# Kernel tuning notes

Measured on AMD Instinct MI355X. Metric: run time of the kernel, lower is better.

Reference implementation:

```python
import jax, jax.numpy as jnp
import numpy as np

B, N, D, J, L = 8, 2046, 128, 128, 2  # batch, ops, feature len, jobs, blocks
C = N + 2  # ops + appended begin/end rows


def setup_inputs() -> dict:
    key = jax.random.key(0)
    ks = jax.random.split(key, 40)

    def w(k, shape, fan_in):
        return jax.random.normal(k, shape, jnp.float32) / np.float32(np.sqrt(fan_in))

    inp = {}
    inp["operation_features"] = jax.random.normal(ks[0], (B, N, D), jnp.float32)
    inp["same_type_mask"] = (jax.random.uniform(ks[1], (B, N, N)) > 0.5).astype(jnp.float32)
    inp["relations"] = jax.random.randint(ks[2], (B, N, 2), 0, N, jnp.int32)
    inp["begins_idx"] = jax.random.randint(ks[3], (B, J), 0, N, jnp.int32)
    inp["ends_idx"] = jax.random.randint(ks[4], (B, J), 0, N, jnp.int32)
    # begin_end_init params
    inp["init_bp_w"] = w(ks[5], (D, D), D); inp["init_bp_b"] = jnp.zeros((D,), jnp.float32)
    inp["init_ep_w"] = w(ks[6], (D, D), D); inp["init_ep_b"] = jnp.zeros((D,), jnp.float32)
    # per-block params, stacked on leading L axis
    inp["be_bp_w"] = w(ks[7], (L, D, D), D); inp["be_bp_b"] = jnp.zeros((L, D), jnp.float32)
    inp["be_ep_w"] = w(ks[8], (L, D, D), D); inp["be_ep_b"] = jnp.zeros((L, D), jnp.float32)
    inp["seq_mix_w"] = w(ks[9], (L, 3 * D, D), 3 * D); inp["seq_mix_b"] = jnp.zeros((L, D), jnp.float32)
    inp["attn_w_w"] = w(ks[10], (L, D, 3 * D), D); inp["attn_w_b"] = jnp.zeros((L, 3 * D), jnp.float32)
    inp["score_w"] = w(ks[11], (L, 2 * D), 2 * D); inp["score_b"] = jnp.zeros((L,), jnp.float32)
    inp["attn_out_w"] = w(ks[12], (L, D, D), D); inp["attn_out_b"] = jnp.zeros((L, D), jnp.float32)
    inp["mix_w"] = w(ks[13], (L, 2 * D, D), 2 * D); inp["mix_b"] = jnp.zeros((L, D), jnp.float32)
    return inp


def _begin_end(ops, begins_idx, ends_idx, bp_w, bp_b, ep_w, ep_b):
    gb = jnp.take_along_axis(ops, begins_idx[..., None], axis=1)  # [B,J,D]
    ge = jnp.take_along_axis(ops, ends_idx[..., None], axis=1)
    begin = jnp.mean(gb @ bp_w + bp_b, axis=1)  # [B,D]
    end = jnp.mean(ge @ ep_w + ep_b, axis=1)
    return begin, end


def _forward(operation_features, same_type_mask,
             init_bp_w, init_bp_b, init_ep_w, init_ep_b,
             be_bp_w, be_bp_b, be_ep_w, be_ep_b,
             seq_mix_w, seq_mix_b, attn_w_w, attn_w_b,
             score_w, score_b, attn_out_w, attn_out_b,
             mix_w, mix_b, relations, begins_idx, ends_idx):
    begin, end = _begin_end(operation_features, begins_idx, ends_idx,
                            init_bp_w, init_bp_b, init_ep_w, init_ep_b)
    feats = jnp.concatenate([operation_features, begin[:, None], end[:, None]], axis=1)  # [B,C,D]
    # -1 sentinels point to appended begin/end rows
    rel_p = jnp.where(relations[..., 0] == -1, N, relations[..., 0])  # [B,N]
    rel_s = jnp.where(relations[..., 1] == -1, N + 1, relations[..., 1])
    mask = jnp.zeros((B, C, C), jnp.float32)
    mask = mask.at[:, :N, :N].set(same_type_mask)
    mask = mask.at[:, N, N].set(1.0).at[:, N + 1, N + 1].set(1.0)

    for l in range(L):
        # --- OperationTimeRelationEncoder ---
        pred = jnp.take_along_axis(feats, rel_p[..., None], axis=1)  # [B,N,D]
        succ = jnp.take_along_axis(feats, rel_s[..., None], axis=1)
        mixed = jnp.concatenate([feats[:, :N], pred, succ], axis=-1) @ seq_mix_w[l] + seq_mix_b[l]
        b2, e2 = _begin_end(feats, begins_idx, ends_idx,
                            be_bp_w[l], be_bp_b[l], be_ep_w[l], be_ep_b[l])
        seq_feats = jnp.concatenate([mixed, b2[:, None], e2[:, None]], axis=1)  # [B,C,D]
        # --- SelfAttention (GAT-style concat score) ---
        qkv = feats @ attn_w_w[l] + attn_w_b[l]
        q, k, v = jnp.split(qkv, 3, axis=-1)  # each [B,C,D]
        wq, wk = score_w[l][:D], score_w[l][D:]
        # score(concat(q_i, k_j)) = q_i.wq + k_j.wk + b, then LeakyReLU
        scores = jax.nn.leaky_relu((q @ wq)[:, :, None] + (k @ wk)[:, None, :] + score_b[l])  # [B,C,C]
        attn = jax.nn.softmax(scores * mask, axis=-1)
        weighted = jnp.einsum('bij,bjh->bih', attn, v)  # [B,C,D]
        attn_out = weighted @ attn_out_w[l] + attn_out_b[l]
        # --- block mix ---
        feats = jnp.concatenate([seq_feats, attn_out], axis=-1) @ mix_w[l] + mix_b[l]

    return jnp.mean(feats, axis=1), feats


def reference(operation_features, same_type_mask,
              init_bp_w, init_bp_b, init_ep_w, init_ep_b,
              be_bp_w, be_bp_b, be_ep_w, be_ep_b,
              seq_mix_w, seq_mix_b, attn_w_w, attn_w_b,
              score_w, score_b, attn_out_w, attn_out_b,
              mix_w, mix_b, relations, begins_idx, ends_idx):
    return _forward(operation_features, same_type_mask,
                    init_bp_w, init_bp_b, init_ep_w, init_ep_b,
                    be_bp_w, be_bp_b, be_ep_w, be_ep_b,
                    seq_mix_w, seq_mix_b, attn_w_w, attn_w_b,
                    score_w, score_b, attn_out_w, attn_out_b,
                    mix_w, mix_b, relations, begins_idx, ends_idx)
```

## Files before the change

kernel.cpp:

```cpp
#include <hip/hip_runtime.h>

constexpr int kB = 8;
constexpr int kN = 2046;
constexpr int kC = 2048;
constexpr int kD = 128;
constexpr int kJ = 128;
constexpr int kL = 2;

typedef short bfrag8 __attribute__((ext_vector_type(8)));
typedef float f32x4 __attribute__((ext_vector_type(4)));

__device__ __forceinline__ float bf2f(unsigned short h) {
  union { unsigned u; float f; } x; x.u = ((unsigned)h) << 16; return x.f;
}
__device__ __forceinline__ unsigned short f2bf(float f) {
  union { float f; unsigned u; } x; x.f = f;
  unsigned u = x.u;
  if ((u & 0x7fffffffu) > 0x7f800000u) return (unsigned short)((u >> 16) | 0x40);
  return (unsigned short)((u + 0x7fffu + ((u >> 16) & 1u)) >> 16);
}
__device__ __forceinline__ unsigned short f2bf_fast(float f) {
  union { float f; unsigned u; } x; x.f = f;
  return (unsigned short)((x.u + 0x7fffu + ((x.u >> 16) & 1u)) >> 16);
}
// ... 40 lines not shown
  for (int o = 1; o < 64; o <<= 1) hits += __shfl_xor(hits, o);
  return hits >= 512;
}

constexpr size_t OF_FEATS = 0;
constexpr size_t OF_SEQ   = 2097152;
constexpr size_t OF_ATTN  = 4194304;
constexpr size_t OF_V     = 6291456;
constexpr size_t OF_SQ    = 8388608;
constexpr size_t OF_SK    = 8404992;
constexpr size_t OF_U     = 8421376;
constexpr size_t OF_PART  = 8422400;
constexpr size_t OF_BMIX  = 8423424;
constexpr size_t OF_WT    = 8423680;

constexpr int WT_SEQH = 0;
constexpr int WT_SEQL = 49152;
constexpr int WT_VH   = 98304;
constexpr int WT_VL   = 114688;
constexpr int WT_MIXH = 131072;
constexpr int WT_MIXL = 163840;
constexpr int WT_LS   = 196608;

constexpr int RP_WT   = 640;
constexpr int RP_WF   = RP_WT + 258;
constexpr int RP_UV   = RP_WF + 2;
constexpr int RP_BE   = RP_UV + 16;
constexpr int RP_PART = RP_BE + 1;
constexpr int RP_CAST = RP_PART + 1023;
constexpr int RP_TOT  = RP_CAST + 4092;

__device__ __forceinline__ f32x4 mfma16(bfrag8 a, bfrag8 b, f32x4 c) {
  return __builtin_amdgcn_mfma_f32_16x16x32_bf16(a, b, c, 0, 0, 0);
}

__global__ __launch_bounds__(256) void k_prep(Raw r, unsigned* __restrict__ feats,
                                              unsigned* __restrict__ bits32,
                                              unsigned short* __restrict__ wt,
                                              float* __restrict__ bmix,
                                              float* __restrict__ u2,
                                              float* __restrict__ part) {
  __shared__ __align__(16) char smem[4096];
  int bid = blockIdx.x, t = threadIdx.x;
  bool bf = sniff(r);

  if (bid < RP_WT) {
    int idx = bid * 256 + t;
    int l = idx / 81920;
    int rr = idx - l * 81920;
    const void* src; size_t si; int dH, dL, k, n;
    if (rr < 49152) {
      k = rr >> 7; n = rr & 127;
      src = r.sw; si = (size_t)l * 49152 + (size_t)k * 128 + n;
      dH = l * WT_LS + WT_SEQH; dL = l * WT_LS + WT_SEQL;
    } else if (rr < 65536) {
      int e = rr - 49152; k = e >> 7; n = e & 127;
      src = r.aw; si = (size_t)l * 49152 + (size_t)k * 384 + 256 + n;
      dH = l * WT_LS + WT_VH; dL = l * WT_LS + WT_VL;
    } else {
      int e = rr - 65536; k = e >> 7; n = e & 127;
      src = r.mw; si = (size_t)l * 32768 + (size_t)k * 128 + n;
      dH = l * WT_LS + WT_MIXH; dL = l * WT_LS + WT_MIXL;
    }
    float v = rp(src, si, bf);
    unsigned short h, lo;
    split2(v, h, lo);
// ... 164 lines not shown
      #pragma unroll
      for (int g = 0; g < 32; ++g) {
        int j = g * 64 + lane;
        v[g] = (j < kN) ? mrow[j] : (unsigned short)0;
      }
      #pragma unroll
      for (int g = 0; g < 32; ++g) {
        unsigned long long bm = __ballot(v[g] != 0);
        if (sel_g == g) wacc = sel_hi ? (unsigned)(bm >> 32) : (unsigned)bm;
      }
    } else {
      const unsigned* mrow = (const unsigned*)r.mask + (size_t)rr * kN;
      unsigned v[32];
      #pragma unroll
      for (int g = 0; g < 32; ++g) {
        int j = g * 64 + lane;
        v[g] = (j < kN) ? mrow[j] : 0u;
      }
      #pragma unroll
      for (int g = 0; g < 32; ++g) {
        unsigned long long bm = __ballot(v[g] != 0);
        if (sel_g == g) wacc = sel_hi ? (unsigned)(bm >> 32) : (unsigned)bm;
      }
    }
    bits32[((size_t)b * kC + i) * 64 + lane] = wacc;
  }
}

__global__ __launch_bounds__(256) void k_stage1(Raw r, int l,
    const unsigned* __restrict__ feats, const unsigned short* __restrict__ wt,
    const float* __restrict__ u2, unsigned* __restrict__ seq,
    unsigned short* __restrict__ Vt, float* __restrict__ sq, float* __restrict__ sk)
{
  __shared__ __align__(16) char smem[21504];
  unsigned short (*Ah)[64 * 40] = (unsigned short(*)[64 * 40])smem;
  unsigned short (*Al)[64 * 40] = (unsigned short(*)[64 * 40])(smem + 10240);
  float* su = (float*)(smem + 20480);
  int bid = blockIdx.x, t = threadIdx.x;
  int lane = t & 63, w = t >> 6, m = lane & 15, quad = lane >> 4;
  bool bf = sniff(r);
  const unsigned short* wl = wt + (size_t)l * WT_LS;

  if (bid >= 16) {
    int g = bid - 16;
    bool isv = g >= 256;
    int rb = isv ? g - 256 : g;
    int gr0 = rb * 64;
    int b = gr0 >> 11, r0 = gr0 & 2047;
    int arow = t >> 2, kq = (t & 3) * 8;
    int nl = r0 + arow;
    const unsigned* fb = feats + (size_t)b * kC * kD;
    const unsigned *s0, *s1, *s2;
    if (!isv) {
      int nr = (nl <= kN - 1) ? nl : (kN - 1);
      const int* rel = r.rel + ((size_t)b * kN + nr) * 2;
      int rpd = rel[0], rsc = rel[1];
      int p = (rpd < 0) ? kN : rpd;
      int s = (rsc < 0) ? (kN + 1) : rsc;
      s0 = fb + (size_t)nl * kD;
      s1 = fb + (size_t)p * kD;
      s2 = fb + (size_t)s * kD;
    } else {
      s0 = fb + (size_t)nl * kD; s1 = s0; s2 = s0;
      su[t] = u2[(size_t)l * 272 + t];
    }
    const int K = isv ? 128 : 384;
    const unsigned short* wth = isv ? (wl + WT_VH) : (wl + WT_SEQH);
    const unsigned short* wtl = isv ? (wl + WT_VL) : (wl + WT_SEQL);
    const unsigned short* pbh = wth + (size_t)(w * 2) * 512 + lane * 8;
    const unsigned short* pbl = wtl + (size_t)(w * 2) * 512 + lane * 8;
    float pq = 0.f, pk2 = 0.f;

    auto build = [&](int kb, int buf) {
      int kg = kb + kq;
      const unsigned* sp;
      if (!isv) sp = (kg < 128) ? (s0 + kg) : (kg < 256) ? (s1 + kg - 128) : (s2 + kg - 256);
      else      sp = s0 + kg;
      uint4 U0 = *(const uint4*)sp;
      uint4 U1 = *(const uint4*)(sp + 4);
      if (isv) {
        float f0 = unpackhl(U0.x), f1 = unpackhl(U0.y), f2 = unpackhl(U0.z), f3 = unpackhl(U0.w);
        float f4 = unpackhl(U1.x), f5 = unpackhl(U1.y), f6 = unpackhl(U1.z), f7 = unpackhl(U1.w);
        pq  += f0 * su[kg]     + f1 * su[kg + 1] + f2 * su[kg + 2] + f3 * su[kg + 3]
             + f4 * su[kg + 4] + f5 * su[kg + 5] + f6 * su[kg + 6] + f7 * su[kg + 7];
        pk2 += f0 * su[128 + kg]     + f1 * su[128 + kg + 1] + f2 * su[128 + kg + 2] + f3 * su[128 + kg + 3]
             + f4 * su[128 + kg + 4] + f5 * su[128 + kg + 5] + f6 * su[128 + kg + 6] + f7 * su[128 + kg + 7];
      }
      uint4 ph, pl;
      ph.x = (U0.x & 0xffffu) | (U0.y << 16);
      pl.x = (U0.x >> 16)     | (U0.y & 0xffff0000u);
      ph.y = (U0.z & 0xffffu) | (U0.w << 16);
      pl.y = (U0.z >> 16)     | (U0.w & 0xffff0000u);
      ph.z = (U1.x & 0xffffu) | (U1.y << 16);
      pl.z = (U1.x >> 16)     | (U1.y & 0xffff0000u);
      ph.w = (U1.z & 0xffffu) | (U1.w << 16);
      pl.w = (U1.z >> 16)     | (U1.w & 0xffff0000u);
      *(uint4*)&Ah[buf][arow * 40 + kq] = ph;
      *(uint4*)&Al[buf][arow * 40 + kq] = pl;
    };

    f32x4 acc[4][2];
    #pragma unroll
    for (int mi = 0; mi < 4; ++mi) { acc[mi][0] = {0.f,0.f,0.f,0.f}; acc[mi][1] = {0.f,0.f,0.f,0.f}; }

    __syncthreads();
    build(0, 0);
    __syncthreads();
    for (int kb = 0; kb < K; kb += 32) {
      int cur = (kb >> 5) & 1;
      int kc = kb >> 5;
      bfrag8 bh0 = *(const bfrag8*)(pbh + (size_t)kc * 4096);
      bfrag8 bh1 = *(const bfrag8*)(pbh + (size_t)kc * 4096 + 512);
      bfrag8 bl0 = {}, bl1 = {};
      if (!bf) {
        bl0 = *(const bfrag8*)(pbl + (size_t)kc * 4096);
        bl1 = *(const bfrag8*)(pbl + (size_t)kc * 4096 + 512);
      }
      if (kb + 32 < K) build(kb + 32, cur ^ 1);
      #pragma unroll
      for (int mi = 0; mi < 4; ++mi) {
        bfrag8 ah = *(const bfrag8*)&Ah[cur][(mi * 16 + m) * 40 + quad * 8];
        bfrag8 al = *(const bfrag8*)&Al[cur][(mi * 16 + m) * 40 + quad * 8];
        acc[mi][0] = mfma16(ah, bh0, acc[mi][0]);
        acc[mi][0] = mfma16(al, bh0, acc[mi][0]);
        acc[mi][1] = mfma16(ah, bh1, acc[mi][1]);
        acc[mi][1] = mfma16(al, bh1, acc[mi][1]);
        if (!bf) {
          acc[mi][0] = mfma16(ah, bl0, acc[mi][0]);
          acc[mi][1] = mfma16(ah, bl1, acc[mi][1]);
        }
      }
      __syncthreads();
    }

    int n0 = w * 32 + m;
    if (!isv) {
      float bv0 = rp(r.sb, (size_t)l * 128 + n0, bf);
      float bv1 = rp(r.sb, (size_t)l * 128 + n0 + 16, bf);
      #pragma unroll
      for (int mi = 0; mi < 4; ++mi)
        #pragma unroll
        for (int reg = 0; reg < 4; ++reg) {
          int ra = r0 + mi * 16 + quad * 4 + reg;
          if (ra < kN) {
            seq[((size_t)b * kC + ra) * kD + n0]      = packhl(acc[mi][0][reg] + bv0);
            seq[((size_t)b * kC + ra) * kD + n0 + 16] = packhl(acc[mi][1][reg] + bv1);
          }
        }
    } else {
      float bv0 = rp(r.ab, (size_t)l * 384 + 256 + n0, bf);
      float bv1 = rp(r.ab, (size_t)l * 384 + 256 + n0 + 16, bf);
      unsigned short* vtb = Vt + (size_t)b * 262144;
      #pragma unroll
      for (int mi = 0; mi < 4; ++mi)
        #pragma unroll
        for (int reg = 0; reg < 4; ++reg) {
          int c = r0 + mi * 16 + quad * 4 + reg;
          int kc = c >> 5, cq = (c >> 3) & 3, e8 = c & 7;
          int lp = cq * 16 + m;
          vtb[((kc * 8 + w * 2) * 64 + lp) * 8 + e8]       = f2bf_fast(acc[mi][0][reg] + bv0);
          vtb[((kc * 8 + w * 2 + 1) * 64 + lp) * 8 + e8]   = f2bf_fast(acc[mi][1][reg] + bv1);
        }
      pq  += __shfl_xor(pq, 1);  pq  += __shfl_xor(pq, 2);
      pk2 += __shfl_xor(pk2, 1); pk2 += __shfl_xor(pk2, 2);
      if ((t & 3) == 0) {
        sq[(size_t)b * kC + nl] = pq + u2[(size_t)l * 272 + 256];
        sk[(size_t)b * kC + nl] = pk2;
      }
    }
  } else {
    int rb = bid;
    int b = rb >> 1, sel = rb & 1;
    float* msh = (float*)smem;
    const int* idx = (sel ? r.eidx : r.bidx) + b * kJ;
    const void* wv = sel ? r.bew : r.bbw;
    const void* bb = sel ? r.beb : r.bbb;
    size_t wbase = (size_t)l * kD * kD, bbase = (size_t)l * kD;
    if (t < 128) {
      int d = t;
      const unsigned* fb2 = feats + (size_t)b * kC * kD;
      float acc = 0.f;
      #pragma unroll 4
      for (int j = 0; j < kJ; ++j) acc += unpackhl(fb2[(size_t)idx[j] * kD + d]);
      msh[d] = acc * (1.0f / kJ);
    }
    __syncthreads();
    if (t < 128) {
      int d = t;
      float o;
      if (bf) {
        const unsigned short* wp = (const unsigned short*)wv + wbase + d;
        o = bf2f(((const unsigned short*)bb)[bbase + d]);
        #pragma unroll 8
        for (int k2 = 0; k2 < kD; ++k2) o += msh[k2] * bf2f(wp[(size_t)k2 * kD]);
      } else {
        const float* wp = (const float*)wv + wbase + d;
        o = ((const float*)bb)[bbase + d];
        #pragma unroll 8
        for (int k2 = 0; k2 < kD; ++k2) o += msh[k2] * wp[(size_t)k2 * kD];
      }
      seq[(size_t)b * kC * kD + (size_t)(kN + sel) * kD + d] = packhl(o);
    }
  }
}

__global__ __launch_bounds__(256) void k_attn_pv_mfma(
    const unsigned* __restrict__ bits,
    const float* __restrict__ sq, const float* __restrict__ sk,
    const unsigned short* __restrict__ Vt,
    unsigned* __restrict__ outw)
{
  int b = blockIdx.y;
  int i0 = blockIdx.x * 32;
  int t = threadIdx.x, lane = t & 63, w = t >> 6;

  __shared__ unsigned short pshare[2][1024];
  __shared__ float sklds[kC];
  __shared__ unsigned bitlds[2048];
  __shared__ float ssq[32], smx[32], szv[32];

  const float* skb = sk + (size_t)b * kC;
  #pragma unroll
  for (int q = 0; q < 8; ++q) sklds[q * 256 + t] = skb[q * 256 + t];
  const unsigned* bitrow = bits + ((size_t)b * kC + i0) * 64;
  #pragma unroll
  for (int q = 0; q < 8; ++q) bitlds[q * 256 + t] = bitrow[q * 256 + t];
  if (t < 32) ssq[t] = sq[(size_t)b * kC + i0 + t];
  __syncthreads();

  {
    int rr = t >> 3, seg = t & 7;
    int ig = i0 + rr;
    bool ok = (ig < kN);
    float sqi2 = ssq[rr];
    const unsigned* bw = bitlds + rr * 64 + seg * 8;
    const float* sks = sklds + seg * 256;
    float mx;
    if (ok) {
      float msk = -3e38f;
      #pragma unroll 1
      for (int w8 = 0; w8 < 8; ++w8) {
        unsigned bb = bw[w8];
        #pragma unroll
        for (int q4 = 0; q4 < 8; ++q4) {
          float4 skv = *(const float4*)(sks + w8 * 32 + q4 * 4);
          unsigned nib = bb >> (q4 * 4);
          msk = (nib & 1u) ? fmaxf(msk, skv.x) : msk;
          msk = (nib & 2u) ? fmaxf(msk, skv.y) : msk;
          msk = (nib & 4u) ? fmaxf(msk, skv.z) : msk;
          msk = (nib & 8u) ? fmaxf(msk, skv.w) : msk;
        }
      }
// ... 9 lines not shown
    float zs = 0.f;
    if (ok) {
      #pragma unroll 1
      for (int w8 = 0; w8 < 8; ++w8) {
        unsigned bb = bw[w8];
        #pragma unroll
        for (int q4 = 0; q4 < 8; ++q4) {
          float4 skv = *(const float4*)(sks + w8 * 32 + q4 * 4);
          unsigned nib = bb >> (q4 * 4);
          float s1 = sqi2 + skv.x, l1 = fmaxf(s1, 0.01f * s1);
          float s2 = sqi2 + skv.y, l2 = fmaxf(s2, 0.01f * s2);
          float s3 = sqi2 + skv.z, l3 = fmaxf(s3, 0.01f * s3);
          float s4 = sqi2 + skv.w, l4 = fmaxf(s4, 0.01f * s4);
          zs += (nib & 1u) ? __expf(l1 - mx) : emx;
          zs += (nib & 2u) ? __expf(l2 - mx) : emx;
          zs += (nib & 4u) ? __expf(l3 - mx) : emx;
          zs += (nib & 8u) ? __expf(l4 - mx) : emx;
        }
      }
    } else {
      zs = 256.f * emx;
      if ((ig >> 8) == seg) {
        float s = sqi2 + sklds[ig & (kC - 1)];
        float lr = fmaxf(s, 0.01f * s);
        zs += __expf(lr - mx) - emx;
      }
    }
    #pragma unroll
    for (int d2 = 1; d2 < 8; d2 <<= 1) zs += __shfl_xor(zs, d2);
    if (seg == 0) { smx[rr] = mx; szv[rr] = 1.0f / zs; }
  }
  __syncthreads();

  int f = t >> 1, h = t & 1;
  int mt_b = f >> 6;
  int lb = f & 63;
  int irow_l = mt_b * 16 + (lb & 15);
  int quad_b = lb >> 4;
  int i_g = i0 + irow_l;
  float sqi = ssq[irow_l];
  float mri = smx[irow_l];
  int joff = quad_b * 8 + h * 4;
  bool irow_ok = (i_g < kN);
  const unsigned char* bitb = (const unsigned char*)bitlds + irow_l * 256;

  auto buildP = [&](int k0, int buf) {
    float4 skv = *(const float4*)(sklds + k0 + joff);
    unsigned byte;
    if (irow_ok) {
      byte = bitb[(k0 >> 3) + quad_b];
    } else {
      int d0 = i_g - (k0 + quad_b * 8);
      byte = ((unsigned)d0 < 8u) ? (1u << d0) : 0u;
    }
    unsigned nib = byte >> (h * 4);
    unsigned short us[4];
    float sv[4] = {skv.x, skv.y, skv.z, skv.w};
    #pragma unroll
    for (int dj = 0; dj < 4; ++dj) {
      float s = sqi + sv[dj];
      float lr = fmaxf(s, 0.01f * s);
      float val = ((nib >> dj) & 1u) ? lr : 0.f;
      us[dj] = f2bf_fast(__expf(val - mri));
    }
    uint2 pk;
    pk.x = us[0] | ((unsigned)us[1] << 16);
    pk.y = us[2] | ((unsigned)us[3] << 16);
    *(uint2*)(&pshare[buf][f * 8 + h * 4]) = pk;
  };

  f32x4 acc00 = {0.f, 0.f, 0.f, 0.f}, acc01 = acc00, acc10 = acc00, acc11 = acc00;
  int m = lane & 15, quad = lane >> 4;
  int nbase = w * 32;
  const unsigned short* vtb = Vt + (size_t)b * 262144;
  const unsigned short* p0 = vtb + (size_t)(w * 2) * 512 + lane * 8;
  const unsigned short* p1 = p0 + 512;

  buildP(0, 0);
  bfrag8 b0n = *(const bfrag8*)p0;
  bfrag8 b1n = *(const bfrag8*)p1;
  __syncthreads();

  for (int k0 = 0; k0 < kC; k0 += 32) {
    int cur = (k0 >> 5) & 1;
    bfrag8 bf0 = b0n, bf1 = b1n;
    if (k0 + 32 < kC) {
      size_t off = (size_t)((k0 >> 5) + 1) * 4096;
      b0n = *(const bfrag8*)(p0 + off);
      b1n = *(const bfrag8*)(p1 + off);
    }
    bfrag8 a0 = *(const bfrag8*)(&pshare[cur][(0 * 64 + lane) * 8]);
    bfrag8 a1 = *(const bfrag8*)(&pshare[cur][(1 * 64 + lane) * 8]);
    acc00 = mfma16(a0, bf0, acc00);
    acc01 = mfma16(a0, bf1, acc01);
    acc10 = mfma16(a1, bf0, acc10);
    acc11 = mfma16(a1, bf1, acc11);
    if (k0 + 32 < kC) buildP(k0 + 32, cur ^ 1);
    __syncthreads();
  }

  #pragma unroll
  for (int reg = 0; reg < 4; ++reg) {
    int il_a = quad * 4 + reg;
    int i_a = i0 + il_a;
    int i_b = i_a + 16;
    float za = szv[il_a];
    float zb = szv[il_a + 16];
    unsigned* oa = outw + ((size_t)b * kC + i_a) * kD + nbase + m;
    unsigned* ob = outw + ((size_t)b * kC + i_b) * kD + nbase + m;
    oa[0]  = packhl(acc00[reg] * za);
    oa[16] = packhl(acc01[reg] * za);
    ob[0]  = packhl(acc10[reg] * zb);
    ob[16] = packhl(acc11[reg] * zb);
  }
}

__global__ __launch_bounds__(256) void k_mix64(Raw r, int l,
    const unsigned* __restrict__ seqb, const unsigned* __restrict__ attnw,
    const unsigned short* __restrict__ wt, const float* __restrict__ bmix,
    unsigned* __restrict__ featsOut, void* __restrict__ outx, float* __restrict__ part,
    int mode)
{
  __shared__ __align__(16) char smem[20480];
  unsigned short (*Ah)[64 * 40] = (unsigned short(*)[64 * 40])smem;
  unsigned short (*Al)[64 * 40] = (unsigned short(*)[64 * 40])(smem + 10240);
  constexpr int K = 256;
  int bid = blockIdx.x, t = threadIdx.x;
  int lane = t & 63, w = t >> 6, m = lane & 15, quad = lane >> 4;
  bool bf = sniff(r);
  int gr0 = bid * 64;
  int b = gr0 >> 11;
  int arow = t >> 2, kq = (t & 3) * 8;
  const unsigned* s0 = seqb  + (size_t)(gr0 + arow) * kD;
  const unsigned* s1 = attnw + (size_t)(gr0 + arow) * kD;
  const unsigned short* wth = wt + (size_t)l * WT_LS + WT_MIXH;
  const unsigned short* wtl = wt + (size_t)l * WT_LS + WT_MIXL;
  const unsigned short* pbh = wth + (size_t)(w * 2) * 512 + lane * 8;
  const unsigned short* pbl = wtl + (size_t)(w * 2) * 512 + lane * 8;

  auto build = [&](int kb, int buf) {
    int kg = kb + kq;
    const unsigned* sp = (kg < kD) ? (s0 + kg) : (s1 + kg - kD);
    uint4 U0 = *(const uint4*)sp;
    uint4 U1 = *(const uint4*)(sp + 4);
    uint4 ph, pl;
    ph.x = (U0.x & 0xffffu) | (U0.y << 16);
    pl.x = (U0.x >> 16)     | (U0.y & 0xffff0000u);
    ph.y = (U0.z & 0xffffu) | (U0.w << 16);
    pl.y = (U0.z >> 16)     | (U0.w & 0xffff0000u);
    ph.z = (U1.x & 0xffffu) | (U1.y << 16);
    pl.z = (U1.x >> 16)     | (U1.y & 0xffff0000u);
    ph.w = (U1.z & 0xffffu) | (U1.w << 16);
    pl.w = (U1.z >> 16)     | (U1.w & 0xffff0000u);
    *(uint4*)&Ah[buf][arow * 40 + kq] = ph;
    *(uint4*)&Al[buf][arow * 40 + kq] = pl;
  };

  f32x4 acc[4][2];
  #pragma unroll
  for (int mi = 0; mi < 4; ++mi) { acc[mi][0] = {0.f,0.f,0.f,0.f}; acc[mi][1] = {0.f,0.f,0.f,0.f}; }

  build(0, 0);
  __syncthreads();
  for (int kb = 0; kb < K; kb += 32) {
    int cur = (kb >> 5) & 1;
    int kc = kb >> 5;
    bfrag8 bh0 = *(const bfrag8*)(pbh + (size_t)kc * 4096);
    bfrag8 bh1 = *(const bfrag8*)(pbh + (size_t)kc * 4096 + 512);
    bfrag8 bl0 = {}, bl1 = {};
    if (!bf) {
      bl0 = *(const bfrag8*)(pbl + (size_t)kc * 4096);
      bl1 = *(const bfrag8*)(pbl + (size_t)kc * 4096 + 512);
    }
    if (kb + 32 < K) build(kb + 32, cur ^ 1);
    #pragma unroll
    for (int mi = 0; mi < 4; ++mi) {
      bfrag8 ah = *(const bfrag8*)&Ah[cur][(mi * 16 + m) * 40 + quad * 8];
      bfrag8 al = *(const bfrag8*)&Al[cur][(mi * 16 + m) * 40 + quad * 8];
      acc[mi][0] = mfma16(ah, bh0, acc[mi][0]);
      acc[mi][0] = mfma16(al, bh0, acc[mi][0]);
      acc[mi][1] = mfma16(ah, bh1, acc[mi][1]);
      acc[mi][1] = mfma16(al, bh1, acc[mi][1]);
      if (!bf) {
        acc[mi][0] = mfma16(ah, bl0, acc[mi][0]);
        acc[mi][1] = mfma16(ah, bl1, acc[mi][1]);
      }
    }
    __syncthreads();
  }

  int n0 = w * 32 + m;
  float bv0 = bmix[(size_t)l * kD + n0];
  float bv1 = bmix[(size_t)l * kD + n0 + 16];
  if (mode == 0) {
    #pragma unroll
    for (int mi = 0; mi < 4; ++mi)
      #pragma unroll
      for (int reg = 0; reg < 4; ++reg) {
        size_t row = (size_t)gr0 + mi * 16 + quad * 4 + reg;
        featsOut[row * kD + n0]      = packhl(acc[mi][0][reg] + bv0);
        featsOut[row * kD + n0 + 16] = packhl(acc[mi][1][reg] + bv1);
      }
  } else {
    float sum0 = 0.f, sum1 = 0.f;
    #pragma unroll
    for (int mi = 0; mi < 4; ++mi)
      #pragma unroll
      for (int reg = 0; reg < 4; ++reg) {
        size_t row = (size_t)gr0 + mi * 16 + quad * 4 + reg;
        float v0 = acc[mi][0][reg] + bv0;
        float v1 = acc[mi][1][reg] + bv1;
        if (bf) {
          unsigned short* o = (unsigned short*)outx + 1024;
          o[row * kD + n0]      = f2bf(v0);
          o[row * kD + n0 + 16] = f2bf(v1);
        } else {
          float* o = (float*)outx + 1024;
          o[row * kD + n0]      = v0;
          o[row * kD + n0 + 16] = v1;
        }
        sum0 += v0; sum1 += v1;
      }
    sum0 += __shfl_xor(sum0, 16); sum0 += __shfl_xor(sum0, 32);
    sum1 += __shfl_xor(sum1, 16); sum1 += __shfl_xor(sum1, 32);
    if (quad == 0) {
      atomicAdd(&part[(size_t)b * kD + n0],      sum0);
      atomicAdd(&part[(size_t)b * kD + n0 + 16], sum1);
    }
  }
}

__global__ __launch_bounds__(128) void k_mean(Raw r, const float* __restrict__ part,
                                              void* __restrict__ out) {
  bool bf = sniff(r);
  int b = blockIdx.x, d = threadIdx.x;
  float v = part[(size_t)b * kD + d] * (1.0f / kC);
  if (bf) ((unsigned short*)out)[b * kD + d] = f2bf(v);
  else    ((float*)out)[b * kD + d] = v;
}

extern "C" void kernel_launch(void* const* d_in, const int* in_sizes, int n_in,
                              void* d_out, int out_size, void* d_ws, size_t ws_size,
                              hipStream_t stream) {
  Raw r;
  r.ops = d_in[0];  r.mask = d_in[1];
  r.rel = (const int*)d_in[2]; r.bidx = (const int*)d_in[3]; r.eidx = (const int*)d_in[4];
  r.ibw = d_in[5];  r.ibb = d_in[6];  r.iew = d_in[7];  r.ieb = d_in[8];
  r.bbw = d_in[9];  r.bbb = d_in[10]; r.bew = d_in[11]; r.beb = d_in[12];
  r.sw  = d_in[13]; r.sb  = d_in[14]; r.aw  = d_in[15]; r.ab  = d_in[16];
  r.scw = d_in[17]; r.scb = d_in[18]; r.aow = d_in[19]; r.aob = d_in[20];
  r.mw  = d_in[21]; r.mb  = d_in[22];

  float* ws    = (float*)d_ws;
  unsigned* feats = (unsigned*)(ws + OF_FEATS);
  unsigned* seq   = (unsigned*)(ws + OF_SEQ);
  unsigned* attnw = (unsigned*)(ws + OF_ATTN);
  float* sq    = ws + OF_SQ;
  float* sk    = ws + OF_SK;
  float* u2    = ws + OF_U;
  float* part  = ws + OF_PART;
// ... 17 lines not shown
```

Measured before the change: 432.1 us.

## Load A fragments directly into registers, drop LDS staging in stage1 and mix GEMMs

Reworks the stage1 and mix GEMM kernels so that each wave owns 16 rows and all 128 output columns. Each wave loads its A fragments straight from global memory into registers with one-step prefetch, which removes the shared-memory A tiles and the per-iteration block barriers. The cost is that every wave now reads the full B weight fragments (8 tiles per k-step instead of 2) and holds more accumulator registers. The mean reduction in mix mode is first combined per block through shared memory, which cuts the number of global atomics.

Measured after the change: 490.1 us. 1.13x slower.

```diff
diff --git a/kernel.cpp b/kernel.cpp
--- a/kernel.cpp
+++ b/kernel.cpp
@@ -96,6 +96,9 @@
 
 __device__ __forceinline__ f32x4 mfma16(bfrag8 a, bfrag8 b, f32x4 c) {
   return __builtin_amdgcn_mfma_f32_16x16x32_bf16(a, b, c, 0, 0, 0);
+}
+__device__ __forceinline__ bfrag8 as_frag(uint4 u) {
+  union { uint4 v; bfrag8 f; } x; x.v = u; return x.f;
 }
 
 __global__ __launch_bounds__(256) void k_prep(Raw r, unsigned* __restrict__ feats,
@@ -326,10 +329,7 @@
     const float* __restrict__ u2, unsigned* __restrict__ seq,
     unsigned short* __restrict__ Vt, float* __restrict__ sq, float* __restrict__ sk)
 {
-  __shared__ __align__(16) char smem[21504];
-  unsigned short (*Ah)[64 * 40] = (unsigned short(*)[64 * 40])smem;
-  unsigned short (*Al)[64 * 40] = (unsigned short(*)[64 * 40])(smem + 10240);
-  float* su = (float*)(smem + 20480);
+  __shared__ float shf[288];
   int bid = blockIdx.x, t = threadIdx.x;
   int lane = t & 63, w = t >> 6, m = lane & 15, quad = lane >> 4;
   bool bf = sniff(r);
@@ -341,131 +341,129 @@
     int rb = isv ? g - 256 : g;
     int gr0 = rb * 64;
     int b = gr0 >> 11, r0 = gr0 & 2047;
-    int arow = t >> 2, kq = (t & 3) * 8;
-    int nl = r0 + arow;
+    int grw = r0 + w * 16;
+    int myrow = grw + m;
     const unsigned* fb = feats + (size_t)b * kC * kD;
     const unsigned *s0, *s1, *s2;
     if (!isv) {
-      int nr = (nl <= kN - 1) ? nl : (kN - 1);
+      int nr = (myrow <= kN - 1) ? myrow : (kN - 1);
       const int* rel = r.rel + ((size_t)b * kN + nr) * 2;
       int rpd = rel[0], rsc = rel[1];
       int p = (rpd < 0) ? kN : rpd;
       int s = (rsc < 0) ? (kN + 1) : rsc;
-      s0 = fb + (size_t)nl * kD;
+      s0 = fb + (size_t)myrow * kD;
       s1 = fb + (size_t)p * kD;
       s2 = fb + (size_t)s * kD;
     } else {
-      s0 = fb + (size_t)nl * kD; s1 = s0; s2 = s0;
-      su[t] = u2[(size_t)l * 272 + t];
+      s0 = fb + (size_t)myrow * kD; s1 = s0; s2 = s0;
+      shf[t] = u2[(size_t)l * 272 + t];
+      if (t < 16) shf[256 + t] = u2[(size_t)l * 272 + 256 + t];
+      __syncthreads();
     }
     const int K = isv ? 128 : 384;
-    const unsigned short* wth = isv ? (wl + WT_VH) : (wl + WT_SEQH);
-    const unsigned short* wtl = isv ? (wl + WT_VL) : (wl + WT_SEQL);
-    const unsigned short* pbh = wth + (size_t)(w * 2) * 512 + lane * 8;
-    const unsigned short* pbl = wtl + (size_t)(w * 2) * 512 + lane * 8;
+    const unsigned short* pbh = (isv ? (wl + WT_VH) : (wl + WT_SEQH)) + (size_t)lane * 8;
+    const unsigned short* pbl = (isv ? (wl + WT_VL) : (wl + WT_SEQL)) + (size_t)lane * 8;
+    int kq8 = quad * 8;
     float pq = 0.f, pk2 = 0.f;
 
-    auto build = [&](int kb, int buf) {
-      int kg = kb + kq;
-      const unsigned* sp;
-      if (!isv) sp = (kg < 128) ? (s0 + kg) : (kg < 256) ? (s1 + kg - 128) : (s2 + kg - 256);
-      else      sp = s0 + kg;
-      uint4 U0 = *(const uint4*)sp;
-      uint4 U1 = *(const uint4*)(sp + 4);
+    f32x4 acc[8];
+    #pragma unroll
+    for (int nt = 0; nt < 8; ++nt) acc[nt] = {0.f, 0.f, 0.f, 0.f};
+
+    auto aptr = [&](int kb) -> const unsigned* {
+      int kg = kb + kq8;
+      if (!isv) return (kg < 128) ? (s0 + kg) : (kg < 256) ? (s1 + kg - 128) : (s2 + kg - 256);
+      return s0 + kg;
+    };
+
+    const unsigned* p00 = aptr(0);
+    uint4 A0 = *(const uint4*)p00;
+    uint4 A1 = *(const uint4*)(p00 + 4);
+
+    #pragma unroll 4
+    for (int kb = 0; kb < K; kb += 32) {
+      uint4 N0, N1;
+      bool more = (kb + 32 < K);
+      if (more) {
+        const unsigned* np = aptr(kb + 32);
+        N0 = *(const uint4*)np;
+        N1 = *(const uint4*)(np + 4);
+      }
       if (isv) {
-        float f0 = unpackhl(U0.x), f1 = unpackhl(U0.y), f2 = unpackhl(U0.z), f3 = unpackhl(U0.w);
-        float f4 = unpackhl(U1.x), f5 = unpackhl(U1.y), f6 = unpackhl(U1.z), f7 = unpackhl(U1.w);
-        pq  += f0 * su[kg]     + f1 * su[kg + 1] + f2 * su[kg + 2] + f3 * su[kg + 3]
-             + f4 * su[kg + 4] + f5 * su[kg + 5] + f6 * su[kg + 6] + f7 * su[kg + 7];
-        pk2 += f0 * su[128 + kg]     + f1 * su[128 + kg + 1] + f2 * su[128 + kg + 2] + f3 * su[128 + kg + 3]
-             + f4 * su[128 + kg + 4] + f5 * su[128 + kg + 5] + f6 * su[128 + kg + 6] + f7 * su[128 + kg + 7];
+        int kg = kb + kq8;
+        float f0 = unpackhl(A0.x), f1 = unpackhl(A0.y), f2 = unpackhl(A0.z), f3 = unpackhl(A0.w);
+        float f4 = unpackhl(A1.x), f5 = unpackhl(A1.y), f6 = unpackhl(A1.z), f7 = unpackhl(A1.w);
+        const float* uqv = shf + kg;
+        const float* ukv = shf + 128 + kg;
+        pq  += f0 * uqv[0] + f1 * uqv[1] + f2 * uqv[2] + f3 * uqv[3]
+             + f4 * uqv[4] + f5 * uqv[5] + f6 * uqv[6] + f7 * uqv[7];
+        pk2 += f0 * ukv[0] + f1 * ukv[1] + f2 * ukv[2] + f3 * ukv[3]
+             + f4 * ukv[4] + f5 * ukv[5] + f6 * ukv[6] + f7 * ukv[7];
       }
       uint4 ph, pl;
-      ph.x = (U0.x & 0xffffu) | (U0.y << 16);
-      pl.x = (U0.x >> 16)     | (U0.y & 0xffff0000u);
-      ph.y = (U0.z & 0xffffu) | (U0.w << 16);
-      pl.y = (U0.z >> 16)     | (U0.w & 0xffff0000u);
-      ph.z = (U1.x & 0xffffu) | (U1.y << 16);
-      pl.z = (U1.x >> 16)     | (U1.y & 0xffff0000u);
-      ph.w = (U1.z & 0xffffu) | (U1.w << 16);
-      pl.w = (U1.z >> 16)     | (U1.w & 0xffff0000u);
-      *(uint4*)&Ah[buf][arow * 40 + kq] = ph;
-      *(uint4*)&Al[buf][arow * 40 + kq] = pl;
-    };
-
-    f32x4 acc[4][2];
-    #pragma unroll
-    for (int mi = 0; mi < 4; ++mi) { acc[mi][0] = {0.f,0.f,0.f,0.f}; acc[mi][1] = {0.f,0.f,0.f,0.f}; }
-
-    __syncthreads();
-    build(0, 0);
-    __syncthreads();
-    for (int kb = 0; kb < K; kb += 32) {
-      int cur = (kb >> 5) & 1;
+      ph.x = (A0.x & 0xffffu) | (A0.y << 16);
+      pl.x = (A0.x >> 16)     | (A0.y & 0xffff0000u);
+      ph.y = (A0.z & 0xffffu) | (A0.w << 16);
+      pl.y = (A0.z >> 16)     | (A0.w & 0xffff0000u);
+      ph.z = (A1.x & 0xffffu) | (A1.y << 16);
+      pl.z = (A1.x >> 16)     | (A1.y & 0xffff0000u);
+      ph.w = (A1.z & 0xffffu) | (A1.w << 16);
+      pl.w = (A1.z >> 16)     | (A1.w & 0xffff0000u);
+      bfrag8 ah = as_frag(ph), al = as_frag(pl);
       int kc = kb >> 5;
-      bfrag8 bh0 = *(const bfrag8*)(pbh + (size_t)kc * 4096);
-      bfrag8 bh1 = *(const bfrag8*)(pbh + (size_t)kc * 4096 + 512);
-      bfrag8 bl0 = {}, bl1 = {};
+      const unsigned short* bbp = pbh + (size_t)kc * 4096;
+      #pragma unroll
+      for (int nt = 0; nt < 8; ++nt) {
+        bfrag8 bh = *(const bfrag8*)(bbp + nt * 512);
+        acc[nt] = mfma16(ah, bh, acc[nt]);
+        acc[nt] = mfma16(al, bh, acc[nt]);
+      }
       if (!bf) {
-        bl0 = *(const bfrag8*)(pbl + (size_t)kc * 4096);
-        bl1 = *(const bfrag8*)(pbl + (size_t)kc * 4096 + 512);
-      }
-      if (kb + 32 < K) build(kb + 32, cur ^ 1);
-      #pragma unroll
-      for (int mi = 0; mi < 4; ++mi) {
-        bfrag8 ah = *(const bfrag8*)&Ah[cur][(mi * 16 + m) * 40 + quad * 8];
-        bfrag8 al = *(const bfrag8*)&Al[cur][(mi * 16 + m) * 40 + quad * 8];
-        acc[mi][0] = mfma16(ah, bh0, acc[mi][0]);
-        acc[mi][0] = mfma16(al, bh0, acc[mi][0]);
-        acc[mi][1] = mfma16(ah, bh1, acc[mi][1]);
-        acc[mi][1] = mfma16(al, bh1, acc[mi][1]);
-        if (!bf) {
-          acc[mi][0] = mfma16(ah, bl0, acc[mi][0]);
-          acc[mi][1] = mfma16(ah, bl1, acc[mi][1]);
-        }
-      }
-      __syncthreads();
-    }
-
-    int n0 = w * 32 + m;
+        const unsigned short* blp = pbl + (size_t)kc * 4096;
+        #pragma unroll
+        for (int nt = 0; nt < 8; ++nt) {
+          bfrag8 bl = *(const bfrag8*)(blp + nt * 512);
+          acc[nt] = mfma16(ah, bl, acc[nt]);
+        }
+      }
+      if (more) { A0 = N0; A1 = N1; }
+    }
+
     if (!isv) {
-      float bv0 = rp(r.sb, (size_t)l * 128 + n0, bf);
-      float bv1 = rp(r.sb, (size_t)l * 128 + n0 + 16, bf);
-      #pragma unroll
-      for (int mi = 0; mi < 4; ++mi)
+      #pragma unroll
+      for (int nt = 0; nt < 8; ++nt) {
+        float bv = rp(r.sb, (size_t)l * 128 + nt * 16 + m, bf);
         #pragma unroll
         for (int reg = 0; reg < 4; ++reg) {
-          int ra = r0 + mi * 16 + quad * 4 + reg;
-          if (ra < kN) {
-            seq[((size_t)b * kC + ra) * kD + n0]      = packhl(acc[mi][0][reg] + bv0);
-            seq[((size_t)b * kC + ra) * kD + n0 + 16] = packhl(acc[mi][1][reg] + bv1);
-          }
-        }
+          int ra = grw + quad * 4 + reg;
+          if (ra < kN)
+            seq[((size_t)b * kC + ra) * kD + nt * 16 + m] = packhl(acc[nt][reg] + bv);
+        }
+      }
     } else {
-      float bv0 = rp(r.ab, (size_t)l * 384 + 256 + n0, bf);
-      float bv1 = rp(r.ab, (size_t)l * 384 + 256 + n0 + 16, bf);
       unsigned short* vtb = Vt + (size_t)b * 262144;
       #pragma unroll
-      for (int mi = 0; mi < 4; ++mi)
+      for (int nt = 0; nt < 8; ++nt) {
+        float bv = rp(r.ab, (size_t)l * 384 + 256 + nt * 16 + m, bf);
         #pragma unroll
         for (int reg = 0; reg < 4; ++reg) {
-          int c = r0 + mi * 16 + quad * 4 + reg;
-          int kc = c >> 5, cq = (c >> 3) & 3, e8 = c & 7;
-          int lp = cq * 16 + m;
-          vtb[((kc * 8 + w * 2) * 64 + lp) * 8 + e8]       = f2bf_fast(acc[mi][0][reg] + bv0);
-          vtb[((kc * 8 + w * 2 + 1) * 64 + lp) * 8 + e8]   = f2bf_fast(acc[mi][1][reg] + bv1);
-        }
-      pq  += __shfl_xor(pq, 1);  pq  += __shfl_xor(pq, 2);
-      pk2 += __shfl_xor(pk2, 1); pk2 += __shfl_xor(pk2, 2);
-      if ((t & 3) == 0) {
-        sq[(size_t)b * kC + nl] = pq + u2[(size_t)l * 272 + 256];
-        sk[(size_t)b * kC + nl] = pk2;
+          int c = grw + quad * 4 + reg;
+          int kcc = c >> 5, e8 = c & 7;
+          int lv = ((c >> 3) & 3) * 16 + m;
+          vtb[((size_t)(kcc * 8 + nt) * 64 + lv) * 8 + e8] = f2bf_fast(acc[nt][reg] + bv);
+        }
+      }
+      pq  += __shfl_xor(pq, 16);  pq  += __shfl_xor(pq, 32);
+      pk2 += __shfl_xor(pk2, 16); pk2 += __shfl_xor(pk2, 32);
+      if (quad == 0) {
+        sq[(size_t)b * kC + grw + m] = pq + shf[256];
+        sk[(size_t)b * kC + grw + m] = pk2;
       }
     }
   } else {
     int rb = bid;
     int b = rb >> 1, sel = rb & 1;
-    float* msh = (float*)smem;
+    float* msh = shf;
     const int* idx = (sel ? r.eidx : r.bidx) + b * kJ;
     const void* wv = sel ? r.bew : r.bbw;
     const void* bb = sel ? r.beb : r.bbb;
@@ -676,111 +674,113 @@
     unsigned* __restrict__ featsOut, void* __restrict__ outx, float* __restrict__ part,
     int mode)
 {
-  __shared__ __align__(16) char smem[20480];
-  unsigned short (*Ah)[64 * 40] = (unsigned short(*)[64 * 40])smem;
-  unsigned short (*Al)[64 * 40] = (unsigned short(*)[64 * 40])(smem + 10240);
+  __shared__ float rsm[512];
   constexpr int K = 256;
   int bid = blockIdx.x, t = threadIdx.x;
   int lane = t & 63, w = t >> 6, m = lane & 15, quad = lane >> 4;
   bool bf = sniff(r);
   int gr0 = bid * 64;
   int b = gr0 >> 11;
-  int arow = t >> 2, kq = (t & 3) * 8;
-  const unsigned* s0 = seqb  + (size_t)(gr0 + arow) * kD;
-  const unsigned* s1 = attnw + (size_t)(gr0 + arow) * kD;
-  const unsigned short* wth = wt + (size_t)l * WT_LS + WT_MIXH;
-  const unsigned short* wtl = wt + (size_t)l * WT_LS + WT_MIXL;
-  const unsigned short* pbh = wth + (size_t)(w * 2) * 512 + lane * 8;
-  const unsigned short* pbl = wtl + (size_t)(w * 2) * 512 + lane * 8;
-
-  auto build = [&](int kb, int buf) {
-    int kg = kb + kq;
-    const unsigned* sp = (kg < kD) ? (s0 + kg) : (s1 + kg - kD);
-    uint4 U0 = *(const uint4*)sp;
-    uint4 U1 = *(const uint4*)(sp + 4);
+  int grw = gr0 + w * 16;
+  int myrow = grw + m;
+  const unsigned* s0 = seqb  + (size_t)myrow * kD;
+  const unsigned* s1 = attnw + (size_t)myrow * kD;
+  const unsigned short* pbh = wt + (size_t)l * WT_LS + WT_MIXH + (size_t)lane * 8;
+  const unsigned short* pbl = wt + (size_t)l * WT_LS + WT_MIXL + (size_t)lane * 8;
+  int kq8 = quad * 8;
+
+  f32x4 acc[8];
+  #pragma unroll
+  for (int nt = 0; nt < 8; ++nt) acc[nt] = {0.f, 0.f, 0.f, 0.f};
+
+  auto aptr = [&](int kb) -> const unsigned* {
+    int kg = kb + kq8;
+    return (kg < kD) ? (s0 + kg) : (s1 + kg - kD);
+  };
+
+  const unsigned* p00 = aptr(0);
+  uint4 A0 = *(const uint4*)p00;
+  uint4 A1 = *(const uint4*)(p00 + 4);
+
+  #pragma unroll 4
+  for (int kb = 0; kb < K; kb += 32) {
+    uint4 N0, N1;
+    bool more = (kb + 32 < K);
+    if (more) {
+      const unsigned* np = aptr(kb + 32);
+      N0 = *(const uint4*)np;
+      N1 = *(const uint4*)(np + 4);
+    }
     uint4 ph, pl;
-    ph.x = (U0.x & 0xffffu) | (U0.y << 16);
-    pl.x = (U0.x >> 16)     | (U0.y & 0xffff0000u);
-    ph.y = (U0.z & 0xffffu) | (U0.w << 16);
-    pl.y = (U0.z >> 16)     | (U0.w & 0xffff0000u);
-    ph.z = (U1.x & 0xffffu) | (U1.y << 16);
-    pl.z = (U1.x >> 16)     | (U1.y & 0xffff0000u);
-    ph.w = (U1.z & 0xffffu) | (U1.w << 16);
-    pl.w = (U1.z >> 16)     | (U1.w & 0xffff0000u);
-    *(uint4*)&Ah[buf][arow * 40 + kq] = ph;
-    *(uint4*)&Al[buf][arow * 40 + kq] = pl;
-  };
-
-  f32x4 acc[4][2];
-  #pragma unroll
-  for (int mi = 0; mi < 4; ++mi) { acc[mi][0] = {0.f,0.f,0.f,0.f}; acc[mi][1] = {0.f,0.f,0.f,0.f}; }
-
-  build(0, 0);
-  __syncthreads();
-  for (int kb = 0; kb < K; kb += 32) {
-    int cur = (kb >> 5) & 1;
+    ph.x = (A0.x & 0xffffu) | (A0.y << 16);
+    pl.x = (A0.x >> 16)     | (A0.y & 0xffff0000u);
+    ph.y = (A0.z & 0xffffu) | (A0.w << 16);
+    pl.y = (A0.z >> 16)     | (A0.w & 0xffff0000u);
+    ph.z = (A1.x & 0xffffu) | (A1.y << 16);
+    pl.z = (A1.x >> 16)     | (A1.y & 0xffff0000u);
+    ph.w = (A1.z & 0xffffu) | (A1.w << 16);
+    pl.w = (A1.z >> 16)     | (A1.w & 0xffff0000u);
+    bfrag8 ah = as_frag(ph), al = as_frag(pl);
     int kc = kb >> 5;
-    bfrag8 bh0 = *(const bfrag8*)(pbh + (size_t)kc * 4096);
-    bfrag8 bh1 = *(const bfrag8*)(pbh + (size_t)kc * 4096 + 512);
-    bfrag8 bl0 = {}, bl1 = {};
+    const unsigned short* bbp = pbh + (size_t)kc * 4096;
+    #pragma unroll
+    for (int nt = 0; nt < 8; ++nt) {
+      bfrag8 bh = *(const bfrag8*)(bbp + nt * 512);
+      acc[nt] = mfma16(ah, bh, acc[nt]);
+      acc[nt] = mfma16(al, bh, acc[nt]);
+    }
     if (!bf) {
-      bl0 = *(const bfrag8*)(pbl + (size_t)kc * 4096);
-      bl1 = *(const bfrag8*)(pbl + (size_t)kc * 4096 + 512);
-    }
-    if (kb + 32 < K) build(kb + 32, cur ^ 1);
-    #pragma unroll
-    for (int mi = 0; mi < 4; ++mi) {
-      bfrag8 ah = *(const bfrag8*)&Ah[cur][(mi * 16 + m) * 40 + quad * 8];
-      bfrag8 al = *(const bfrag8*)&Al[cur][(mi * 16 + m) * 40 + quad * 8];
-      acc[mi][0] = mfma16(ah, bh0, acc[mi][0]);
-      acc[mi][0] = mfma16(al, bh0, acc[mi][0]);
-      acc[mi][1] = mfma16(ah, bh1, acc[mi][1]);
-      acc[mi][1] = mfma16(al, bh1, acc[mi][1]);
-      if (!bf) {
-        acc[mi][0] = mfma16(ah, bl0, acc[mi][0]);
-        acc[mi][1] = mfma16(ah, bl1, acc[mi][1]);
-      }
-    }
-    __syncthreads();
+      const unsigned short* blp = pbl + (size_t)kc * 4096;
+      #pragma unroll
+      for (int nt = 0; nt < 8; ++nt) {
+        bfrag8 bl = *(const bfrag8*)(blp + nt * 512);
+        acc[nt] = mfma16(ah, bl, acc[nt]);
+      }
+    }
+    if (more) { A0 = N0; A1 = N1; }
   }
 
-  int n0 = w * 32 + m;
-  float bv0 = bmix[(size_t)l * kD + n0];
-  float bv1 = bmix[(size_t)l * kD + n0 + 16];
   if (mode == 0) {
     #pragma unroll
-    for (int mi = 0; mi < 4; ++mi)
+    for (int nt = 0; nt < 8; ++nt) {
+      float bv = bmix[(size_t)l * kD + nt * 16 + m];
       #pragma unroll
       for (int reg = 0; reg < 4; ++reg) {
-        size_t row = (size_t)gr0 + mi * 16 + quad * 4 + reg;
-        featsOut[row * kD + n0]      = packhl(acc[mi][0][reg] + bv0);
-        featsOut[row * kD + n0 + 16] = packhl(acc[mi][1][reg] + bv1);
-      }
+        size_t row = (size_t)grw + quad * 4 + reg;
+        featsOut[row * kD + nt * 16 + m] = packhl(acc[nt][reg] + bv);
+      }
+    }
   } else {
-    float sum0 = 0.f, sum1 = 0.f;
+    float csum[8];
     #pragma unroll
-    for (int mi = 0; mi < 4; ++mi)
+    for (int nt = 0; nt < 8; ++nt) {
+      float bv = bmix[(size_t)l * kD + nt * 16 + m];
+      float s = 0.f;
       #pragma unroll
       for (int reg = 0; reg < 4; ++reg) {
-        size_t row = (size_t)gr0 + mi * 16 + quad * 4 + reg;
-        float v0 = acc[mi][0][reg] + bv0;
-        float v1 = acc[mi][1][reg] + bv1;
+        size_t row = (size_t)grw + quad * 4 + reg;
+        float v = acc[nt][reg] + bv;
         if (bf) {
           unsigned short* o = (unsigned short*)outx + 1024;
-          o[row * kD + n0]      = f2bf(v0);
-          o[row * kD + n0 + 16] = f2bf(v1);
+          o[row * kD + nt * 16 + m] = f2bf(v);
         } else {
           float* o = (float*)outx + 1024;
-          o[row * kD + n0]      = v0;
-          o[row * kD + n0 + 16] = v1;
-        }
-        sum0 += v0; sum1 += v1;
-      }
-    sum0 += __shfl_xor(sum0, 16); sum0 += __shfl_xor(sum0, 32);
-    sum1 += __shfl_xor(sum1, 16); sum1 += __shfl_xor(sum1, 32);
+          o[row * kD + nt * 16 + m] = v;
+        }
+        s += v;
+      }
+      s += __shfl_xor(s, 16);
+      s += __shfl_xor(s, 32);
+      csum[nt] = s;
+    }
     if (quad == 0) {
-      atomicAdd(&part[(size_t)b * kD + n0],      sum0);
-      atomicAdd(&part[(size_t)b * kD + n0 + 16], sum1);
+      #pragma unroll
+      for (int nt = 0; nt < 8; ++nt) rsm[w * 128 + nt * 16 + m] = csum[nt];
+    }
+    __syncthreads();
+    if (t < 128) {
+      float tot = rsm[t] + rsm[128 + t] + rsm[256 + t] + rsm[384 + t];
+      atomicAdd(&part[(size_t)b * kD + t], tot);
     }
   }
 }
```

## Split attention PV over key dimension per wave with LDS reduction

Applied to the files above, without the earlier changes.

Restructures the attention P·V kernel so each of the four waves owns a quarter of the key range and computes all 128 output columns, building its P fragments in registers rather than through a shared double-buffered LDS tile. The per-iteration block-wide barrier is removed, and each wave now issues 16 MFMAs per step instead of 4. Partial accumulators are summed through a padded LDS buffer with serialized per-wave accumulation before the normalized output is written. In exchange it uses far more accumulator registers (64 floats per lane), drops the explicit V prefetch, and adds a serialized reduction.

Result: slower. 442.0 us (+2.3%).

```diff
diff --git a/kernel.cpp b/kernel.cpp
--- a/kernel.cpp
+++ b/kernel.cpp
@@ -96,6 +96,9 @@
 
 __device__ __forceinline__ f32x4 mfma16(bfrag8 a, bfrag8 b, f32x4 c) {
   return __builtin_amdgcn_mfma_f32_16x16x32_bf16(a, b, c, 0, 0, 0);
+}
+__device__ __forceinline__ bfrag8 as_frag(uint4 u) {
+  union { uint4 v; bfrag8 f; } x; x.v = u; return x.f;
 }
 
 __global__ __launch_bounds__(256) void k_prep(Raw r, unsigned* __restrict__ feats,
@@ -508,10 +511,10 @@
   int i0 = blockIdx.x * 32;
   int t = threadIdx.x, lane = t & 63, w = t >> 6;
 
-  __shared__ unsigned short pshare[2][1024];
   __shared__ float sklds[kC];
   __shared__ unsigned bitlds[2048];
   __shared__ float ssq[32], smx[32], szv[32];
+  __shared__ float redu[32 * 130];
 
   const float* skb = sk + (size_t)b * kC;
   #pragma unroll
@@ -587,86 +590,90 @@
   }
   __syncthreads();
 
-  int f = t >> 1, h = t & 1;
-  int mt_b = f >> 6;
-  int lb = f & 63;
-  int irow_l = mt_b * 16 + (lb & 15);
-  int quad_b = lb >> 4;
-  int i_g = i0 + irow_l;
-  float sqi = ssq[irow_l];
-  float mri = smx[irow_l];
-  int joff = quad_b * 8 + h * 4;
-  bool irow_ok = (i_g < kN);
-  const unsigned char* bitb = (const unsigned char*)bitlds + irow_l * 256;
-
-  auto buildP = [&](int k0, int buf) {
-    float4 skv = *(const float4*)(sklds + k0 + joff);
-    unsigned byte;
-    if (irow_ok) {
-      byte = bitb[(k0 >> 3) + quad_b];
-    } else {
-      int d0 = i_g - (k0 + quad_b * 8);
-      byte = ((unsigned)d0 < 8u) ? (1u << d0) : 0u;
-    }
-    unsigned nib = byte >> (h * 4);
-    unsigned short us[4];
-    float sv[4] = {skv.x, skv.y, skv.z, skv.w};
+  int m = lane & 15, quad = lane >> 4;
+  float sq0 = ssq[m],      mx0 = smx[m];
+  float sq1 = ssq[16 + m], mx1 = smx[16 + m];
+  int ig0 = i0 + m, ig1 = i0 + 16 + m;
+  bool ok0 = ig0 < kN, ok1 = ig1 < kN;
+  const unsigned char* bitb0 = (const unsigned char*)bitlds + m * 256;
+  const unsigned char* bitb1 = (const unsigned char*)bitlds + (16 + m) * 256;
+  const unsigned short* vtb = Vt + (size_t)b * 262144 + (size_t)lane * 8;
+
+  f32x4 acc[2][8];
+  #pragma unroll
+  for (int it = 0; it < 2; ++it)
     #pragma unroll
-    for (int dj = 0; dj < 4; ++dj) {
-      float s = sqi + sv[dj];
-      float lr = fmaxf(s, 0.01f * s);
-      float val = ((nib >> dj) & 1u) ? lr : 0.f;
-      us[dj] = f2bf_fast(__expf(val - mri));
-    }
-    uint2 pk;
-    pk.x = us[0] | ((unsigned)us[1] << 16);
-    pk.y = us[2] | ((unsigned)us[3] << 16);
-    *(uint2*)(&pshare[buf][f * 8 + h * 4]) = pk;
-  };
-
-  f32x4 acc00 = {0.f, 0.f, 0.f, 0.f}, acc01 = acc00, acc10 = acc00, acc11 = acc00;
-  int m = lane & 15, quad = lane >> 4;
+    for (int nt = 0; nt < 8; ++nt) acc[it][nt] = {0.f, 0.f, 0.f, 0.f};
+
+  #pragma unroll 2
+  for (int s = 0; s < 16; ++s) {
+    int j0 = w * 512 + s * 32;
+    int jb = j0 + quad * 8;
+    float4 skv0 = *(const float4*)(sklds + jb);
+    float4 skv1 = *(const float4*)(sklds + jb + 4);
+    unsigned byte0, byte1;
+    if (ok0) byte0 = bitb0[jb >> 3];
+    else { int d0 = ig0 - jb; byte0 = ((unsigned)d0 < 8u) ? (1u << d0) : 0u; }
+    if (ok1) byte1 = bitb1[jb >> 3];
+    else { int d1 = ig1 - jb; byte1 = ((unsigned)d1 < 8u) ? (1u << d1) : 0u; }
+    float sv[8] = {skv0.x, skv0.y, skv0.z, skv0.w, skv1.x, skv1.y, skv1.z, skv1.w};
+    unsigned short u0[8], u1[8];
+    #pragma unroll
+    for (int e = 0; e < 8; ++e) {
+      float sa = sq0 + sv[e];
+      float la = fmaxf(sa, 0.01f * sa);
+      float va = ((byte0 >> e) & 1u) ? la : 0.f;
+      u0[e] = f2bf_fast(__expf(va - mx0));
+      float sb2 = sq1 + sv[e];
+      float lb2 = fmaxf(sb2, 0.01f * sb2);
+      float vb = ((byte1 >> e) & 1u) ? lb2 : 0.f;
+      u1[e] = f2bf_fast(__expf(vb - mx1));
+    }
+    uint4 pa0, pa1;
+    pa0.x = u0[0] | ((unsigned)u0[1] << 16); pa0.y = u0[2] | ((unsigned)u0[3] << 16);
+    pa0.z = u0[4] | ((unsigned)u0[5] << 16); pa0.w = u0[6] | ((unsigned)u0[7] << 16);
+    pa1.x = u1[0] | ((unsigned)u1[1] << 16); pa1.y = u1[2] | ((unsigned)u1[3] << 16);
+    pa1.z = u1[4] | ((unsigned)u1[5] << 16); pa1.w = u1[6] | ((unsigned)u1[7] << 16);
+    bfrag8 a0 = as_frag(pa0), a1 = as_frag(pa1);
+    const unsigned short* vp = vtb + (size_t)(j0 >> 5) * 4096;
+    #pragma unroll
+    for (int nt = 0; nt < 8; ++nt) {
+      bfrag8 bv = *(const bfrag8*)(vp + nt * 512);
+      acc[0][nt] = mfma16(a0, bv, acc[0][nt]);
+      acc[1][nt] = mfma16(a1, bv, acc[1][nt]);
+    }
+  }
+
+  for (int ww = 0; ww < 4; ++ww) {
+    if (w == ww) {
+      #pragma unroll
+      for (int it = 0; it < 2; ++it)
+        #pragma unroll
+        for (int nt = 0; nt < 8; ++nt)
+          #pragma unroll
+          for (int reg = 0; reg < 4; ++reg) {
+            int row = it * 16 + quad * 4 + reg;
+            int col = nt * 16 + m;
+            if (ww == 0) redu[row * 130 + col] = acc[it][nt][reg];
+            else         redu[row * 130 + col] += acc[it][nt][reg];
+          }
+    }
+    __syncthreads();
+  }
+
   int nbase = w * 32;
-  const unsigned short* vtb = Vt + (size_t)b * 262144;
-  const unsigned short* p0 = vtb + (size_t)(w * 2) * 512 + lane * 8;
-  const unsigned short* p1 = p0 + 512;
-
-  buildP(0, 0);
-  bfrag8 b0n = *(const bfrag8*)p0;
-  bfrag8 b1n = *(const bfrag8*)p1;
-  __syncthreads();
-
-  for (int k0 = 0; k0 < kC; k0 += 32) {
-    int cur = (k0 >> 5) & 1;
-    bfrag8 bf0 = b0n, bf1 = b1n;
-    if (k0 + 32 < kC) {
-      size_t off = (size_t)((k0 >> 5) + 1) * 4096;
-      b0n = *(const bfrag8*)(p0 + off);
-      b1n = *(const bfrag8*)(p1 + off);
-    }
-    bfrag8 a0 = *(const bfrag8*)(&pshare[cur][(0 * 64 + lane) * 8]);
-    bfrag8 a1 = *(const bfrag8*)(&pshare[cur][(1 * 64 + lane) * 8]);
-    acc00 = mfma16(a0, bf0, acc00);
-    acc01 = mfma16(a0, bf1, acc01);
-    acc10 = mfma16(a1, bf0, acc10);
-    acc11 = mfma16(a1, bf1, acc11);
-    if (k0 + 32 < kC) buildP(k0 + 32, cur ^ 1);
-    __syncthreads();
-  }
-
   #pragma unroll
   for (int reg = 0; reg < 4; ++reg) {
-    int il_a = quad * 4 + reg;
-    int i_a = i0 + il_a;
-    int i_b = i_a + 16;
-    float za = szv[il_a];
-    float zb = szv[il_a + 16];
-    unsigned* oa = outw + ((size_t)b * kC + i_a) * kD + nbase + m;
-    unsigned* ob = outw + ((size_t)b * kC + i_b) * kD + nbase + m;
-    oa[0]  = packhl(acc00[reg] * za);
-    oa[16] = packhl(acc01[reg] * za);
-    ob[0]  = packhl(acc10[reg] * zb);
-    ob[16] = packhl(acc11[reg] * zb);
+    int ra = quad * 4 + reg;
+    int rb2 = ra + 16;
+    float za = szv[ra];
+    float zb = szv[rb2];
+    unsigned* oa = outw + ((size_t)b * kC + i0 + ra) * kD + nbase + m;
+    unsigned* ob = outw + ((size_t)b * kC + i0 + rb2) * kD + nbase + m;
+    oa[0]  = packhl(redu[ra * 130 + nbase + m] * za);
+    oa[16] = packhl(redu[ra * 130 + nbase + m + 16] * za);
+    ob[0]  = packhl(redu[rb2 * 130 + nbase + m] * zb);
+    ob[16] = packhl(redu[rb2 * 130 + nbase + m + 16] * zb);
   }
 }
 
```
